# Kernel tuning notes

Hardware: AMD Instinct MI355X
Metric: run time of the kernel (lower is better)

Reference implementation:

```python
import jax, jax.numpy as jnp
import numpy as np

B, S, T, H, L, V = 32, 64, 32, 512, 2, 32000
BOS = 1


def _gru_cell(x, h, Wih, Whh, bih, bhh):
    # torch GRU gate order: r, z, n
    gi = x @ Wih.T + bih
    gh = h @ Whh.T + bhh
    i_r, i_z, i_n = jnp.split(gi, 3, axis=-1)
    h_r, h_z, h_n = jnp.split(gh, 3, axis=-1)
    r = jax.nn.sigmoid(i_r + h_r)
    z = jax.nn.sigmoid(i_z + h_z)
    n = jnp.tanh(i_n + r * h_n)
    return (1.0 - z) * n + z * h


def setup_inputs() -> dict:
    key = jax.random.key(0)
    ks = jax.random.split(key, 20)
    sd = 0.02
    inp = {
        "encoder_outputs": jax.random.normal(ks[0], (B, S, H), jnp.float32),
        "encoder_hidden": jax.random.normal(ks[1], (L, B, H), jnp.float32),
        "target_tensor": jax.random.randint(ks[2], (B, T), 0, V, jnp.int32),
        "emb": jax.random.normal(ks[3], (V, H), jnp.float32) * sd,
        "Wa": jax.random.normal(ks[4], (H, H * L), jnp.float32) * sd,
        "ba": jnp.zeros((H,), jnp.float32),
        "Ua": jax.random.normal(ks[5], (H, H), jnp.float32) * sd,
        "bua": jnp.zeros((H,), jnp.float32),
        "Va": jax.random.normal(ks[6], (1, H), jnp.float32) * sd,
        "bva": jnp.zeros((1,), jnp.float32),
        "gru0_Wih": jax.random.normal(ks[7], (3 * H, 2 * H), jnp.float32) * sd,
        "gru0_Whh": jax.random.normal(ks[8], (3 * H, H), jnp.float32) * sd,
        "gru0_bih": jnp.zeros((3 * H,), jnp.float32),
        "gru0_bhh": jnp.zeros((3 * H,), jnp.float32),
        "gru1_Wih": jax.random.normal(ks[9], (3 * H, H), jnp.float32) * sd,
        "gru1_Whh": jax.random.normal(ks[10], (3 * H, H), jnp.float32) * sd,
        "gru1_bih": jnp.zeros((3 * H,), jnp.float32),
        "gru1_bhh": jnp.zeros((3 * H,), jnp.float32),
        "outW": jax.random.normal(ks[11], (V, H), jnp.float32) * sd,
        "outb": jnp.zeros((V,), jnp.float32),
    }
    return inp


def reference(encoder_outputs, encoder_hidden, target_tensor, emb, Wa, ba, Ua, bua, Va, bva,
              gru0_Wih, gru0_Whh, gru0_bih, gru0_bhh,
              gru1_Wih, gru1_Whh, gru1_bih, gru1_bhh, outW, outb):
    Tlen = target_tensor.shape[1]
    # Ua(keys) is constant across decode steps -> precompute (same math)
    Ukeys = encoder_outputs @ Ua.T + bua  # [B,S,H]

    def step(carry, _):
        hidden, tok = carry  # hidden [L,B,H], tok [B] int
        x = emb[tok]  # [B,H]  (dropout_p=0 -> identity)
        query = jnp.transpose(hidden, (1, 0, 2)).reshape(hidden.shape[1], -1)  # [B,L*H]
        q = query @ Wa.T + ba  # [B,H]
        s = jnp.tanh(q[:, None, :] + Ukeys)  # [B,S,H]
        scores = jnp.squeeze(s @ Va.T, -1) + bva[0]  # [B,S]
        w = jax.nn.softmax(scores, axis=-1)  # [B,S]
        context = jnp.einsum('bs,bsh->bh', w, encoder_outputs)  # [B,H]
        gin = jnp.concatenate([x, context], axis=-1)  # [B,2H]
        h0 = _gru_cell(gin, hidden[0], gru0_Wih, gru0_Whh, gru0_bih, gru0_bhh)
        h1 = _gru_cell(h0, hidden[1], gru1_Wih, gru1_Whh, gru1_bih, gru1_bhh)
        new_hidden = jnp.stack([h0, h1], axis=0)
        logits = h1 @ outW.T + outb  # [B,V]
        tok_next = jnp.argmax(logits, axis=-1)  # greedy (topk(1), detached)
        return (new_hidden, tok_next), (logits, w)

    tok0 = jnp.full((encoder_outputs.shape[0],), BOS, dtype=jnp.int32)
    (hidden, _), (logits, attn) = jax.lax.scan(step, (encoder_hidden, tok0), None, length=Tlen)
    logits = jnp.transpose(logits, (1, 0, 2))  # [B,T,V]
    attn = jnp.transpose(attn, (1, 0, 2))      # [B,T,S]
    log_probs = jax.nn.log_softmax(logits, axis=-1)
    return (log_probs, hidden, attn)
```

## Files before the change

kernel.cpp:

```cpp
#include <hip/hip_runtime.h>
#include <cstdint>
#include <cstddef>

#define B_  32
#define S_  64
#define T_  32
#define H_  512
#define V_  32000
#define H3_ 1536

#define OFF_HID   0
#define OFF_H0N   32768
#define OFF_H1N   49152
#define OFF_UK    65536
#define OFF_Q     1114112
#define OFF_GIN   1130496
#define OFF_GI0   1163264
#define OFF_GH0   1212416
#define OFF_GI1   1261568
#define OFF_GH1   1310720
#define OFF_LSE   1359872
#define OFF_SMAX  1360896
#define OFF_SSUM  1424896
#define OFF_SIDX  1488896

#define OUT_LOGP  0
#define OUT_HIDN  32768000
#define OUT_ATTN  32800768

__device__ __forceinline__ float sigm(float x){ return 1.f/(1.f + __expf(-x)); }
__device__ __forceinline__ float tanh_(float x){ float e = __expf(2.f*x); return 1.f - 2.f/(e + 1.f); }
__device__ __forceinline__ float dot4(float4 w, float4 h, float a){
  a = fmaf(w.x,h.x,a); a = fmaf(w.y,h.y,a); a = fmaf(w.z,h.z,a); a = fmaf(w.w,h.w,a); return a;
}

__global__ __launch_bounds__(256) void k_init(const float* __restrict__ ehid, float* __restrict__ ws)
{
  int i = blockIdx.x*256 + threadIdx.x;
  if (i < 2*B_*H_) ws[OFF_HID + i] = ehid[i];
  if (i < B_*H_)   ws[OFF_Q + i] = 0.f;
}

__global__ __launch_bounds__(256) void k_ukeys(const float* __restrict__ enc, const float* __restrict__ Ua,
                                               const float* __restrict__ bua, float* __restrict__ ws)
{
  __shared__ float As[16][65];
  __shared__ float Bs[16][65];
  int rb = blockIdx.x >> 3, cb = blockIdx.x & 7;
  int row0 = rb*64, col0 = cb*64;
  int tid = threadIdx.x;
  int tx = tid & 15, ty = tid >> 4;
  int lr = tid >> 2, lk = (tid & 3)*4;
  float acc[4][4] = {{0.f}};
  for (int k0 = 0; k0 < 512; k0 += 16){
    float4 a4 = *(const float4*)(enc + (size_t)(row0+lr)*512 + k0 + lk);
    As[lk+0][lr]=a4.x; As[lk+1][lr]=a4.y; As[lk+2][lr]=a4.z; As[lk+3][lr]=a4.w;
    float4 b4 = *(const float4*)(Ua + (size_t)(col0+lr)*512 + k0 + lk);
    Bs[lk+0][lr]=b4.x; Bs[lk+1][lr]=b4.y; Bs[lk+2][lr]=b4.z; Bs[lk+3][lr]=b4.w;
    __syncthreads();
    #pragma unroll
    for (int kk = 0; kk < 16; kk++){
      float a[4], bb[4];
      #pragma unroll
      for (int i=0;i<4;i++) a[i] = As[kk][ty*4+i];
      #pragma unroll
      for (int j=0;j<4;j++) bb[j] = Bs[kk][tx*4+j];
      #pragma unroll
      for (int i=0;i<4;i++)
        #pragma unroll
        for (int j=0;j<4;j++) acc[i][j] = fmaf(a[i], bb[j], acc[i][j]);
    }
    __syncthreads();
  }
  #pragma unroll
  for (int i=0;i<4;i++){
    int r = row0 + ty*4 + i;
    #pragma unroll
    for (int j=0;j<4;j++){
      int c = col0 + tx*4 + j;
      ws[OFF_UK + (size_t)r*512 + c] = acc[i][j] + bua[c];
    }
  }
}

__device__ void stats_reduce(const float* __restrict__ ws, int b, int tid,
                             float* rm, float* rs, int* ri, int& token, float& lse)
{
  float m = -1e30f, s = 0.f; int idx = 0x7fffffff;
  for (int c = tid; c < 2000; c += 256){
    float cm = ws[OFF_SMAX + c*32 + b];
    float cs = ws[OFF_SSUM + c*32 + b];
    int   ci = ((const int*)ws)[OFF_SIDX + c*32 + b];
    float M = fmaxf(m, cm);
    s = s*__expf(m - M) + cs*__expf(cm - M);
    if (cm > m || (cm == m && ci < idx)) idx = ci;
    m = M;
  }
  rm[tid]=m; rs[tid]=s; ri[tid]=idx;
  __syncthreads();
  for (int off=128; off>0; off>>=1){
    if (tid < off){
      float m1=rm[tid], s1=rs[tid]; int i1=ri[tid];
      float m2=rm[tid+off], s2=rs[tid+off]; int i2=ri[tid+off];
      float M=fmaxf(m1,m2);
      rs[tid] = s1*__expf(m1-M) + s2*__expf(m2-M);
      ri[tid] = (m2 > m1 || (m2==m1 && i2<i1)) ? i2 : i1;
      rm[tid] = M;
    }
    __syncthreads();
  }
  token = ri[0];
  lse = rm[0] + logf(rs[0]);
}

__global__ __launch_bounds__(256) void k_attn(int t, const float* __restrict__ emb,
    const float* __restrict__ enc, const float* __restrict__ Va, const float* __restrict__ bva,
    float* __restrict__ ws, float* __restrict__ out)
{
  int b = blockIdx.x, tid = threadIdx.x;
  for (int i = tid; i < 6144; i += 256) ws[OFF_GI0 + b*6144 + i] = 0.f;

  __shared__ float rm[256], rs[256];
  __shared__ int   ri[256];
  __shared__ float sQ[512], sVa[512], sW[64];

  int token; float lse;
  if (t > 0){
    stats_reduce(ws, b, tid, rm, rs, ri, token, lse);
    if (tid == 0) ws[OFF_LSE + (t-1)*32 + b] = lse;
  } else {
    token = 1;
  }
  for (int i = tid; i < 512; i += 256) ws[OFF_GIN + b*1024 + i] = emb[(size_t)token*512 + i];
  for (int i = tid; i < 512; i += 256){ sQ[i] = ws[OFF_Q + b*512 + i]; sVa[i] = Va[i]; }
  __syncthreads();

  int lane = tid & 63, wv = tid >> 6;
  float bv = bva[0];
  for (int si = 0; si < 16; si++){
    int s = wv*16 + si;
    const float* uk = ws + OFF_UK + ((size_t)b*64 + s)*512 + lane*8;
    const float* qq = sQ + lane*8;
    const float* vv = sVa + lane*8;
    float4 u0 = *(const float4*)(uk), u1 = *(const float4*)(uk+4);
    float p = tanh_(qq[0]+u0.x)*vv[0] + tanh_(qq[1]+u0.y)*vv[1]
            + tanh_(qq[2]+u0.z)*vv[2] + tanh_(qq[3]+u0.w)*vv[3]
            + tanh_(qq[4]+u1.x)*vv[4] + tanh_(qq[5]+u1.y)*vv[5]
            + tanh_(qq[6]+u1.z)*vv[6] + tanh_(qq[7]+u1.w)*vv[7];
    for (int off=32; off; off>>=1) p += __shfl_xor(p, off);
    if (lane == 0) sW[s] = p + bv;
  }
  __syncthreads();
  if (wv == 0){
    float sc = sW[lane];
    float m = sc;
    for (int off=32; off; off>>=1) m = fmaxf(m, __shfl_xor(m, off));
    float e = __expf(sc - m);
    float Ssum = e;
    for (int off=32; off; off>>=1) Ssum += __shfl_xor(Ssum, off);
    float wgt = e / Ssum;
    sW[lane] = wgt;
    out[OUT_ATTN + ((size_t)b*T_ + t)*S_ + lane] = wgt;
  }
  __syncthreads();
  float c0 = 0.f, c1 = 0.f;
  for (int s = 0; s < 64; s++){
    float wgt = sW[s];
    const float* er = enc + ((size_t)b*64 + s)*512;
    c0 = fmaf(wgt, er[tid], c0);
    c1 = fmaf(wgt, er[tid+256], c1);
  }
  ws[OFF_GIN + b*1024 + 512 + tid]       = c0;
  ws[OFF_GIN + b*1024 + 512 + tid + 256] = c1;
}

__global__ __launch_bounds__(256) void k_gates0(const float* __restrict__ Wih, const float* __restrict__ Whh,
    const float* __restrict__ bih, const float* __restrict__ bhh, float* __restrict__ ws)
{
  int cc = blockIdx.x % 24, ks = blockIdx.x / 24;
  int tid = threadIdx.x;
  if (blockIdx.x < 64) ws[OFF_Q + blockIdx.x*256 + tid] = 0.f;
  __shared__ float gT[256][32];
  __shared__ float hT[128][32];
  {
    int b = tid & 31, kq = tid >> 5;
    for (int it = 0; it < 8; it++){
      int k = it*32 + kq*4;
      float4 v = *(const float4*)(ws + OFF_GIN + b*1024 + ks*256 + k);
      gT[k+0][b]=v.x; gT[k+1][b]=v.y; gT[k+2][b]=v.z; gT[k+3][b]=v.w;
    }
    for (int it = 0; it < 4; it++){
      int k = it*32 + kq*4;
      float4 v = *(const float4*)(ws + OFF_HID + b*512 + ks*128 + k);
      hT[k+0][b]=v.x; hT[k+1][b]=v.y; hT[k+2][b]=v.z; hT[k+3][b]=v.w;
    }
  }
  __syncthreads();
  int lane = tid & 63, wv = tid >> 6;
  int b = lane & 31, ch = lane >> 5;
  int c0 = cc*64 + wv*16 + ch*8;
  float ai[8] = {0,0,0,0,0,0,0,0}, ah[8] = {0,0,0,0,0,0,0,0};
  for (int j = 0; j < 64; j++){
    float4 h4 = { gT[j*4+0][b], gT[j*4+1][b], gT[j*4+2][b], gT[j*4+3][b] };
    #pragma unroll
    for (int vv = 0; vv < 8; vv++){
      float4 w4 = *(const float4*)(Wih + (size_t)(c0+vv)*1024 + ks*256 + j*4);
      ai[vv] = dot4(w4, h4, ai[vv]);
    }
  }
  for (int j = 0; j < 32; j++){
    float4 h4 = { hT[j*4+0][b], hT[j*4+1][b], hT[j*4+2][b], hT[j*4+3][b] };
    #pragma unroll
    for (int vv = 0; vv < 8; vv++){
      float4 w4 = *(const float4*)(Whh + (size_t)(c0+vv)*512 + ks*128 + j*4);
      ah[vv] = dot4(w4, h4, ah[vv]);
    }
  }
  #pragma unroll
  for (int vv = 0; vv < 8; vv++){
    float a = ai[vv] + (ks==0 ? bih[c0+vv] : 0.f);
    float h = ah[vv] + (ks==0 ? bhh[c0+vv] : 0.f);
    atomicAdd(ws + OFF_GI0 + b*H3_ + c0 + vv, a);
    atomicAdd(ws + OFF_GH0 + b*H3_ + c0 + vv, h);
  }
}

__global__ __launch_bounds__(256) void k_gates1(const float* __restrict__ Wih, const float* __restrict__ Whh,
    const float* __restrict__ bih, const float* __restrict__ bhh, float* __restrict__ ws)
{
  int cc = blockIdx.x % 24, ks = blockIdx.x / 24;
  int tid = threadIdx.x;
  __shared__ float h0T[128][32];
  __shared__ float h1T[128][32];
  for (int i = tid; i < 4096; i += 256){
    int b = i & 31, kk = i >> 5;
    int k = ks*128 + kk;
    float ir = ws[OFF_GI0 + b*H3_ + k],         hr = ws[OFF_GH0 + b*H3_ + k];
    float iz = ws[OFF_GI0 + b*H3_ + 512 + k],   hz = ws[OFF_GH0 + b*H3_ + 512 + k];
    float in_= ws[OFF_GI0 + b*H3_ + 1024 + k],  hn = ws[OFF_GH0 + b*H3_ + 1024 + k];
    float r = sigm(ir + hr), z = sigm(iz + hz);
    float n = tanh_(in_ + r*hn);
    float h0 = (1.f - z)*n + z*ws[OFF_HID + b*512 + k];
    h0T[kk][b] = h0;
    if (cc == 0) ws[OFF_H0N + b*512 + k] = h0;
  }
  {
    int b = tid & 31, kq = tid >> 5;
    for (int it = 0; it < 4; it++){
      int k = it*32 + kq*4;
      float4 v = *(const float4*)(ws + OFF_HID + 16384 + b*512 + ks*128 + k);
      h1T[k+0][b]=v.x; h1T[k+1][b]=v.y; h1T[k+2][b]=v.z; h1T[k+3][b]=v.w;
    }
  }
  __syncthreads();
  int lane = tid & 63, wv = tid >> 6;
  int b = lane & 31, ch = lane >> 5;
  int c0 = cc*64 + wv*16 + ch*8;
  float ai[8] = {0,0,0,0,0,0,0,0}, ah[8] = {0,0,0,0,0,0,0,0};
  for (int j = 0; j < 32; j++){
    float4 a4 = { h0T[j*4+0][b], h0T[j*4+1][b], h0T[j*4+2][b], h0T[j*4+3][b] };
    float4 b4 = { h1T[j*4+0][b], h1T[j*4+1][b], h1T[j*4+2][b], h1T[j*4+3][b] };
    #pragma unroll
    for (int vv = 0; vv < 8; vv++){
      float4 wi = *(const float4*)(Wih + (size_t)(c0+vv)*512 + ks*128 + j*4);
      ai[vv] = dot4(wi, a4, ai[vv]);
      float4 wh = *(const float4*)(Whh + (size_t)(c0+vv)*512 + ks*128 + j*4);
      ah[vv] = dot4(wh, b4, ah[vv]);
    }
  }
  #pragma unroll
  for (int vv = 0; vv < 8; vv++){
    float a = ai[vv] + (ks==0 ? bih[c0+vv] : 0.f);
    float h = ah[vv] + (ks==0 ? bhh[c0+vv] : 0.f);
    atomicAdd(ws + OFF_GI1 + b*H3_ + c0 + vv, a);
    atomicAdd(ws + OFF_GH1 + b*H3_ + c0 + vv, h);
  }
}

__global__ __launch_bounds__(256) void k_hq(int init, const float* __restrict__ Wa,
    const float* __restrict__ ba, float* __restrict__ ws)
{
  int cc = blockIdx.x & 7, ks = blockIdx.x >> 3;
  int tid = threadIdx.x;
  __shared__ float qT[256][32];
  if (!init && ks >= 2){
    for (int i = tid; i < 8192; i += 256){
      int b = i & 31, kk = i >> 5;
      int k = (ks - 2)*256 + kk;
      float ir = ws[OFF_GI1 + b*H3_ + k],        hr = ws[OFF_GH1 + b*H3_ + k];
      float iz = ws[OFF_GI1 + b*H3_ + 512 + k],  hz = ws[OFF_GH1 + b*H3_ + 512 + k];
      float in_= ws[OFF_GI1 + b*H3_ + 1024 + k], hn = ws[OFF_GH1 + b*H3_ + 1024 + k];
      float r = sigm(ir+hr), z = sigm(iz+hz);
      float n = tanh_(in_ + r*hn);
      float h1 = (1.f - z)*n + z*ws[OFF_HID + 16384 + b*512 + k];
      qT[kk][b] = h1;
      if (cc == 0) ws[OFF_H1N + b*512 + k] = h1;
    }
  } else {
    int b = tid & 31, kq = tid >> 5;
    const float* src;
    if (init) src = ws + OFF_HID + (ks >> 1)*16384 + (ks & 1)*256;
    else      src = ws + OFF_H0N + ks*256;
    for (int it = 0; it < 8; it++){
      int k = it*32 + kq*4;
      float4 v = *(const float4*)(src + b*512 + k);
      qT[k+0][b]=v.x; qT[k+1][b]=v.y; qT[k+2][b]=v.z; qT[k+3][b]=v.w;
    }
  }
  if (!init && ks < 2 && cc == 0){
    for (int i = tid; i < 8192; i += 256){
      int b = i & 31, kk = i >> 5;
      ws[OFF_HID + b*512 + ks*256 + kk] = ws[OFF_H0N + b*512 + ks*256 + kk];
    }
  }
  __syncthreads();
  int lane = tid & 63, wv = tid >> 6;
  int b = lane & 31, ch = lane >> 5;
  int c0 = cc*64 + wv*16 + ch*8;
  float acc[8] = {0,0,0,0,0,0,0,0};
  for (int j = 0; j < 64; j++){
    float4 h4 = { qT[j*4+0][b], qT[j*4+1][b], qT[j*4+2][b], qT[j*4+3][b] };
    #pragma unroll
    for (int vv = 0; vv < 8; vv++){
      float4 w4 = *(const float4*)(Wa + (size_t)(c0+vv)*1024 + ks*256 + j*4);
      acc[vv] = dot4(w4, h4, acc[vv]);
    }
  }
  #pragma unroll
  for (int vv = 0; vv < 8; vv++)
    atomicAdd(ws + OFF_Q + b*512 + c0 + vv, acc[vv] + (ks==0 ? ba[c0+vv] : 0.f));
}

__global__ __launch_bounds__(256) void k_logits(int t, const float* __restrict__ outW,
    const float* __restrict__ outb, float* __restrict__ ws, float* __restrict__ out)
{
  __shared__ float hT[512][32];
  int tid = threadIdx.x;
  if (blockIdx.x == 0){
    for (int i = tid; i < 16384; i += 256) ws[OFF_HID + 16384 + i] = ws[OFF_H1N + i];
  }
  {
    int b = tid & 31, kq = tid >> 5;
    for (int it = 0; it < 16; it++){
      int k = it*32 + kq*4;
      float4 v = *(const float4*)(ws + OFF_H1N + b*512 + k);
      hT[k+0][b]=v.x; hT[k+1][b]=v.y; hT[k+2][b]=v.z; hT[k+3][b]=v.w;
    }
  }
  __syncthreads();
  int lane = tid & 63, wv = tid >> 6;
  int b = lane & 31, vh = lane >> 5;
  int v0 = blockIdx.x*64 + wv*16 + vh*8;
  const float* w0 = outW + (size_t)v0*512;
  float acc[8] = {0,0,0,0,0,0,0,0};
  for (int j = 0; j < 128; j++){
    float4 h4 = { hT[j*4+0][b], hT[j*4+1][b], hT[j*4+2][b], hT[j*4+3][b] };
    #pragma unroll
    for (int vv = 0; vv < 8; vv++){
      float4 w4 = *(const float4*)(w0 + vv*512 + j*4);
      acc[vv] = dot4(w4, h4, acc[vv]);
    }
  }
  float vals[8];
  #pragma unroll
  for (int vv = 0; vv < 8; vv++) vals[vv] = acc[vv] + outb[v0+vv];
  float* orow = out + OUT_LOGP + ((size_t)b*T_ + t)*V_ + v0;
  float4 o0 = {vals[0],vals[1],vals[2],vals[3]};
  float4 o1 = {vals[4],vals[5],vals[6],vals[7]};
  *(float4*)(orow)     = o0;
  *(float4*)(orow + 4) = o1;
  float m = vals[0]; int mi = v0;
  #pragma unroll
  for (int vv = 1; vv < 8; vv++){ if (vals[vv] > m){ m = vals[vv]; mi = v0+vv; } }
  float se = 0.f;
  #pragma unroll
  for (int vv = 0; vv < 8; vv++) se += __expf(vals[vv] - m);
  float m2 = __shfl_xor(m, 32);
  float s2 = __shfl_xor(se, 32);
  int   i2 = __shfl_xor(mi, 32);
  float M = fmaxf(m, m2);
  se = se*__expf(m-M) + s2*__expf(m2-M);
  mi = (m2 > m || (m2 == m && i2 < mi)) ? i2 : mi;
  if (lane < 32){
    int chunk = blockIdx.x*4 + wv;
    ws[OFF_SMAX + chunk*32 + b] = M;
    ws[OFF_SSUM + chunk*32 + b] = se;
    ((int*)ws)[OFF_SIDX + chunk*32 + b] = mi;
  }
}

__global__ __launch_bounds__(256) void k_finstats(float* __restrict__ ws)
{
  __shared__ float rm[256], rs[256];
  __shared__ int   ri[256];
  int b = blockIdx.x; int token; float lse;
  stats_reduce(ws, b, threadIdx.x, rm, rs, ri, token, lse);
  if (threadIdx.x == 0) ws[OFF_LSE + 31*32 + b] = lse;
}

__global__ __launch_bounds__(256) void k_finout(const float* __restrict__ ws, float* __restrict__ out)
{
  if (blockIdx.x < 16000){
    size_t base = (size_t)blockIdx.x*2048 + (size_t)threadIdx.x*8;
    int b = (int)(base / ((size_t)T_*V_));
    int t = (int)((base / V_) % T_);
    float lse = ws[OFF_LSE + t*32 + b];
    float4* p = (float4*)(out + base);
    float4 x = p[0], y = p[1];
    x.x-=lse; x.y-=lse; x.z-=lse; x.w-=lse;
    y.x-=lse; y.y-=lse; y.z-=lse; y.w-=lse;
    p[0]=x; p[1]=y;
  } else {
    int i = (blockIdx.x - 16000)*2048 + threadIdx.x*8;
    const float4* s = (const float4*)(ws + OFF_HID + i);
    float4* d = (float4*)(out + OUT_HIDN + i);
    d[0] = s[0]; d[1] = s[1];
  }
}

extern "C" void kernel_launch(void* const* d_in, const int* in_sizes, int n_in,
                              void* d_out, int out_size, void* d_ws, size_t ws_size,
                              hipStream_t stream)
{
  (void)in_sizes; (void)n_in; (void)out_size; (void)ws_size;
  const float* enc   = (const float*)d_in[0];
  const float* ehid  = (const float*)d_in[1];
  const float* emb   = (const float*)d_in[3];
  const float* Wa    = (const float*)d_in[4];
  const float* ba    = (const float*)d_in[5];
  const float* Ua    = (const float*)d_in[6];
  const float* bua   = (const float*)d_in[7];
  const float* Va    = (const float*)d_in[8];
  const float* bva   = (const float*)d_in[9];
  const float* g0Wih = (const float*)d_in[10];
  const float* g0Whh = (const float*)d_in[11];
  const float* g0bih = (const float*)d_in[12];
  const float* g0bhh = (const float*)d_in[13];
  const float* g1Wih = (const float*)d_in[14];
  const float* g1Whh = (const float*)d_in[15];
  const float* g1bih = (const float*)d_in[16];
  const float* g1bhh = (const float*)d_in[17];
  const float* outW  = (const float*)d_in[18];
  const float* outb  = (const float*)d_in[19];
  float* ws  = (float*)d_ws;
  float* out = (float*)d_out;

  hipLaunchKernelGGL(k_init,   dim3(128), dim3(256), 0, stream, ehid, ws);
  hipLaunchKernelGGL(k_ukeys,  dim3(256), dim3(256), 0, stream, enc, Ua, bua, ws);
  hipLaunchKernelGGL(k_hq,     dim3(32),  dim3(256), 0, stream, 1, Wa, ba, ws);
  for (int t = 0; t < T_; t++){
    hipLaunchKernelGGL(k_attn,   dim3(32),  dim3(256), 0, stream, t, emb, enc, Va, bva, ws, out);
    hipLaunchKernelGGL(k_gates0, dim3(96),  dim3(256), 0, stream, g0Wih, g0Whh, g0bih, g0bhh, ws);
    hipLaunchKernelGGL(k_gates1, dim3(96),  dim3(256), 0, stream, g1Wih, g1Whh, g1bih, g1bhh, ws);
    hipLaunchKernelGGL(k_hq,     dim3(32),  dim3(256), 0, stream, 0, Wa, ba, ws);
    hipLaunchKernelGGL(k_logits, dim3(500), dim3(256), 0, stream, t, outW, outb, ws, out);
  }
  hipLaunchKernelGGL(k_finstats, dim3(32),    dim3(256), 0, stream, ws);
  hipLaunchKernelGGL(k_finout,   dim3(16016), dim3(256), 0, stream, ws, out);
}
```

Before: 7.077 ms.

## Restructure logits GEMV to split K across lanes with permlane-swap reductions

The output-projection kernel now assigns each lane a slice of the hidden dimension instead of one batch row. Each lane computes partial dot products for 4 vocab rows times 32 batches, then reduces across lanes with v_permlane32/16_swap and shuffle butterflies. The hidden state is staged untransposed in shared memory with coalesced float4 copies, and weight rows are read coalesced and double-buffered in registers. The intent is to make the large outW stream fully coalesced and to cut LDS transpose traffic. In exchange it adds heavy register pressure (a 4x32 accumulator array, with launch bounds of 2 blocks per SM) and many cross-lane reduction instructions.

```diff
diff --git a/kernel.cpp b/kernel.cpp
--- a/kernel.cpp
+++ b/kernel.cpp
@@ -331,61 +331,134 @@
     atomicAdd(ws + OFF_Q + b*512 + c0 + vv, acc[vv] + (ks==0 ? ba[c0+vv] : 0.f));
 }
 
-__global__ __launch_bounds__(256) void k_logits(int t, const float* __restrict__ outW,
+#define R_(i) a[(i)>>5][(i)&31]
+__global__ __launch_bounds__(256, 2) void k_logits(int t, const float* __restrict__ outW,
     const float* __restrict__ outb, float* __restrict__ ws, float* __restrict__ out)
 {
-  __shared__ float hT[512][32];
+  __shared__ float hT[32][512];
   int tid = threadIdx.x;
+  {
+    const float4* src = (const float4*)(ws + OFF_H1N);
+    float4* dst = (float4*)(&hT[0][0]);
+    for (int i = tid; i < 4096; i += 256) dst[i] = src[i];
+  }
   if (blockIdx.x == 0){
     for (int i = tid; i < 16384; i += 256) ws[OFF_HID + 16384 + i] = ws[OFF_H1N + i];
   }
-  {
-    int b = tid & 31, kq = tid >> 5;
-    for (int it = 0; it < 16; it++){
-      int k = it*32 + kq*4;
-      float4 v = *(const float4*)(ws + OFF_H1N + b*512 + k);
-      hT[k+0][b]=v.x; hT[k+1][b]=v.y; hT[k+2][b]=v.z; hT[k+3][b]=v.w;
-    }
-  }
-  __syncthreads();
+  __syncthreads();
+
   int lane = tid & 63, wv = tid >> 6;
-  int b = lane & 31, vh = lane >> 5;
-  int v0 = blockIdx.x*64 + wv*16 + vh*8;
-  const float* w0 = outW + (size_t)v0*512;
-  float acc[8] = {0,0,0,0,0,0,0,0};
-  for (int j = 0; j < 128; j++){
-    float4 h4 = { hT[j*4+0][b], hT[j*4+1][b], hT[j*4+2][b], hT[j*4+3][b] };
-    #pragma unroll
-    for (int vv = 0; vv < 8; vv++){
-      float4 w4 = *(const float4*)(w0 + vv*512 + j*4);
-      acc[vv] = dot4(w4, h4, acc[vv]);
-    }
-  }
-  float vals[8];
+  int vbase = blockIdx.x*64 + wv*16;
+  int rsel = lane >> 4;
+  int b0 = (lane & 15)*2;
+
+  float m0=-1e30f, se0=0.f, m1=-1e30f, se1=0.f;
+  int idx0=0x7fffffff, idx1=0x7fffffff;
+
+  const float* hrow = &hT[0][0] + lane*4;
+
+  float4 w[4][2], wn[4][2];
   #pragma unroll
-  for (int vv = 0; vv < 8; vv++) vals[vv] = acc[vv] + outb[v0+vv];
-  float* orow = out + OUT_LOGP + ((size_t)b*T_ + t)*V_ + v0;
-  float4 o0 = {vals[0],vals[1],vals[2],vals[3]};
-  float4 o1 = {vals[4],vals[5],vals[6],vals[7]};
-  *(float4*)(orow)     = o0;
-  *(float4*)(orow + 4) = o1;
-  float m = vals[0]; int mi = v0;
+  for (int r = 0; r < 4; r++){
+    const float* wr = outW + (size_t)(vbase + r)*512 + lane*4;
+    w[r][0] = *(const float4*)(wr);
+    w[r][1] = *(const float4*)(wr + 256);
+  }
+
+  for (int it = 0; it < 4; it++){
+    if (it < 3){
+      #pragma unroll
+      for (int r = 0; r < 4; r++){
+        const float* wr = outW + (size_t)(vbase + (it+1)*4 + r)*512 + lane*4;
+        wn[r][0] = *(const float4*)(wr);
+        wn[r][1] = *(const float4*)(wr + 256);
+      }
+    }
+    float a[4][32];
+    #pragma unroll
+    for (int b = 0; b < 32; b++){
+      float4 h0 = *(const float4*)(hrow + b*512);
+      float4 h1 = *(const float4*)(hrow + b*512 + 256);
+      #pragma unroll
+      for (int r = 0; r < 4; r++){
+        float s = 0.f;
+        s = dot4(w[r][0], h0, s);
+        s = dot4(w[r][1], h1, s);
+        a[r][b] = s;
+      }
+    }
+    #pragma unroll
+    for (int i = 0; i < 64; i++){
+      float x = R_(i), y = R_(i+64);
+      asm volatile("s_nop 1\n\tv_permlane32_swap_b32 %0, %1" : "+v"(x), "+v"(y));
+      R_(i) = x + y;
+    }
+    #pragma unroll
+    for (int i = 0; i < 32; i++){
+      float x = R_(i), y = R_(i+32);
+      asm volatile("s_nop 1\n\tv_permlane16_swap_b32 %0, %1" : "+v"(x), "+v"(y));
+      R_(i) = x + y;
+    }
+    #pragma unroll
+    for (int lb = 3; lb >= 0; lb--){
+      int half = 1 << (lb + 1);
+      bool bit = (lane >> lb) & 1;
+      #pragma unroll
+      for (int i = 0; i < (1 << (lb + 1)); i++){
+        if (i < half){}
+      }
+      #pragma unroll
+      for (int i = 0; i < 16; i++){
+        if (i < half){
+          float keep = bit ? R_(i+half) : R_(i);
+          float send = bit ? R_(i) : R_(i+half);
+          R_(i) = keep + __shfl_xor(send, 1 << lb, 64);
+        }
+      }
+    }
+    int v = vbase + it*4 + rsel;
+    float ob = outb[v];
+    float x0 = R_(0) + ob;
+    float x1 = R_(1) + ob;
+    size_t obase = (size_t)OUT_LOGP + (size_t)b0*(T_*V_) + (size_t)t*V_ + v;
+    out[obase] = x0;
+    out[obase + (size_t)(T_*V_)] = x1;
+    float M0 = fmaxf(m0, x0);
+    se0 = se0*__expf(m0 - M0) + __expf(x0 - M0);
+    if (x0 > m0) idx0 = v;
+    m0 = M0;
+    float M1 = fmaxf(m1, x1);
+    se1 = se1*__expf(m1 - M1) + __expf(x1 - M1);
+    if (x1 > m1) idx1 = v;
+    m1 = M1;
+    #pragma unroll
+    for (int r = 0; r < 4; r++){ w[r][0] = wn[r][0]; w[r][1] = wn[r][1]; }
+  }
+
   #pragma unroll
-  for (int vv = 1; vv < 8; vv++){ if (vals[vv] > m){ m = vals[vv]; mi = v0+vv; } }
-  float se = 0.f;
-  #pragma unroll
-  for (int vv = 0; vv < 8; vv++) se += __expf(vals[vv] - m);
-  float m2 = __shfl_xor(m, 32);
-  float s2 = __shfl_xor(se, 32);
-  int   i2 = __shfl_xor(mi, 32);
-  float M = fmaxf(m, m2);
-  se = se*__expf(m-M) + s2*__expf(m2-M);
-  mi = (m2 > m || (m2 == m && i2 < mi)) ? i2 : mi;
-  if (lane < 32){
+  for (int d = 4; d <= 5; d++){
+    int msk = 1 << d;
+    float m2 = __shfl_xor(m0, msk, 64), s2 = __shfl_xor(se0, msk, 64);
+    int   i2 = __shfl_xor(idx0, msk, 64);
+    float M = fmaxf(m0, m2);
+    se0 = se0*__expf(m0 - M) + s2*__expf(m2 - M);
+    idx0 = (m2 > m0 || (m2 == m0 && i2 < idx0)) ? i2 : idx0;
+    m0 = M;
+    float m3 = __shfl_xor(m1, msk, 64), s3 = __shfl_xor(se1, msk, 64);
+    int   i3 = __shfl_xor(idx1, msk, 64);
+    float N = fmaxf(m1, m3);
+    se1 = se1*__expf(m1 - N) + s3*__expf(m3 - N);
+    idx1 = (m3 > m1 || (m3 == m1 && i3 < idx1)) ? i3 : idx1;
+    m1 = N;
+  }
+  if (lane < 16){
     int chunk = blockIdx.x*4 + wv;
-    ws[OFF_SMAX + chunk*32 + b] = M;
-    ws[OFF_SSUM + chunk*32 + b] = se;
-    ((int*)ws)[OFF_SIDX + chunk*32 + b] = mi;
+    ws[OFF_SMAX + chunk*32 + b0]   = m0;
+    ws[OFF_SMAX + chunk*32 + b0+1] = m1;
+    ws[OFF_SSUM + chunk*32 + b0]   = se0;
+    ws[OFF_SSUM + chunk*32 + b0+1] = se1;
+    ((int*)ws)[OFF_SIDX + chunk*32 + b0]   = idx0;
+    ((int*)ws)[OFF_SIDX + chunk*32 + b0+1] = idx1;
   }
 }
 
```

Result: faster. 5.991 ms (-15.4%).
